# Kernel tuning notes

Measured on AMD Instinct MI355X. Metric: run time of the kernel, lower is better.

## Reference

```python
import jax, jax.numpy as jnp
import numpy as np

BN_EPS = 1e-5

def _l2norm(x, axis):
    # F.normalize: x / max(||x||_2, 1e-12)
    n = jnp.sqrt(jnp.sum(x * x, axis=axis, keepdims=True))
    return x / jnp.maximum(n, 1e-12)

def _psi(x_bhc, w, g, b):
    # 1x1 conv over HW-as-channels: [B,HW,C] x [D,HW] -> [B,D,C]
    y = jnp.einsum('dh,bhc->bdc', w, x_bhc)
    # inference BatchNorm2d with running_mean=0, running_var=1
    scale = g / jnp.sqrt(1.0 + BN_EPS)
    y = y * scale[None, :, None] + b[None, :, None]
    return jax.nn.relu(y)

def setup_inputs() -> dict:
    key = jax.random.key(0)
    ks = jax.random.split(key, 8)
    B, C, H, W, D = 16, 2048, 32, 32, 256
    return {
        'v2l_conv_feature': jax.random.normal(ks[0], (B, C, H, W), jnp.float32),
        'l2v_conv_feature': jax.random.normal(ks[1], (B, C, H, W), jnp.float32),
        'w_v2l': jax.random.normal(ks[2], (D, H * W), jnp.float32) * 0.02,
        'g_v2l': jax.random.uniform(ks[3], (D,), jnp.float32, 0.5, 1.5),
        'b_v2l': jax.random.normal(ks[4], (D,), jnp.float32) * 0.1,
        'w_l2v': jax.random.normal(ks[5], (D, H * W), jnp.float32) * 0.02,
        'g_l2v': jax.random.uniform(ks[6], (D,), jnp.float32, 0.5, 1.5),
        'b_l2v': jax.random.normal(ks[7], (D,), jnp.float32) * 0.1,
    }

def reference(v2l_conv_feature, l2v_conv_feature, w_v2l, g_v2l, b_v2l, w_l2v, g_l2v, b_l2v):
    B, C, H, W = v2l_conv_feature.shape
    HW = H * W
    xv = jnp.transpose(v2l_conv_feature.reshape(B, C, HW), (0, 2, 1))  # [B,HW,C]
    xl = jnp.transpose(l2v_conv_feature.reshape(B, C, HW), (0, 2, 1))  # [B,HW,C]
    v2l_adj = _l2norm(_psi(xv, w_v2l, g_v2l, b_v2l), axis=2)  # [B,D,C], norm over C
    l2v_adj = _l2norm(_psi(xl, w_l2v, g_l2v, b_l2v), axis=1)  # [B,D,C], norm over D
    # Faithful to torch: reshape of the permuted tensor is a raw row-major
    # reinterpretation [B,HW,C] -> [B,C,HW] (NOT a transpose back).
    xv_r = xv.reshape(B, C, HW)
    latent = jnp.einsum('bdc,bch->bdh', v2l_adj, xv_r)          # [B,D,HW]
    latent_n = _l2norm(latent, axis=-1)
    aff = jax.nn.softmax(jnp.einsum('bdh,beh->bde', latent_n, latent_n), axis=-1)  # [B,D,D]
    latent = jnp.einsum('bde,beh->bdh', aff, latent)            # [B,D,HW]
    visible = jnp.einsum('bdc,bdh->bch', l2v_adj, latent)       # [B,C,HW]
    return visible.reshape(B, C, H, W)
```

## Files before the change

### kernel.cpp

```cpp
#include <hip/hip_runtime.h>
#include <hip/hip_bf16.h>

#define BB 16
#define CC 2048
#define HWW 1024
#define DD 256
#define BN_RSQRT 0.9999950000374997f

typedef short bf16x8 __attribute__((ext_vector_type(8)));
typedef float f32x4 __attribute__((ext_vector_type(4)));
typedef unsigned short u16x8 __attribute__((ext_vector_type(8)));
typedef unsigned short u16;

__device__ __forceinline__ unsigned short f2bf(float x) {
    unsigned u = __builtin_bit_cast(unsigned, x);
    unsigned r = u + 0x7FFFu + ((u >> 16) & 1u);
    return (unsigned short)(r >> 16);
}
__device__ __forceinline__ float bf2f(unsigned short h) {
    unsigned u = ((unsigned)h) << 16;
    return __builtin_bit_cast(float, u);
}
__device__ __forceinline__ void split2(float x, unsigned short& hi, unsigned short& lo) {
    hi = f2bf(x);
    lo = f2bf(x - bf2f(hi));
}
__device__ __forceinline__ void split16(const float* v, u16x8& h0, u16x8& h1,
                                        u16x8& l0, u16x8& l1) {
    #pragma unroll
    for (int j = 0; j < 8; ++j) { unsigned short hh, ll; split2(v[j], hh, ll); h0[j] = hh; l0[j] = ll; }
    #pragma unroll
    for (int j = 0; j < 8; ++j) { unsigned short hh, ll; split2(v[8 + j], hh, ll); h1[j] = hh; l1[j] = ll; }
}

struct RegsA { float4 f[4]; u16x8 h[2]; u16x8 l[2]; };
struct RegsB { float4 f[4]; u16x8 h[2]; u16x8 l[2]; };

__global__ __launch_bounds__(256) void split_k(const float* __restrict__ in,
                                               u16* __restrict__ hi, u16* __restrict__ lo,
                                               long long n8) {
    long long i = (long long)blockIdx.x * 256 + threadIdx.x;
    if (i >= n8) return;
    const float4* p = (const float4*)in + i * 2;
    float4 a = p[0], b = p[1];
    float xs[8] = {a.x, a.y, a.z, a.w, b.x, b.y, b.z, b.w};
    u16x8 h, l;
    #pragma unroll
    for (int j = 0; j < 8; ++j) { unsigned short hh, ll; split2(xs[j], hh, ll); h[j] = hh; l[j] = ll; }
    *(u16x8*)(hi + i * 8) = h;
    *(u16x8*)(lo + i * 8) = l;
}

template <int BFMT, int EPI, int FUSE2>
__global__ __launch_bounds__(512, 2) void gemm8(
    const u16* __restrict__ Ah0, const u16* __restrict__ Al0,
    const u16* __restrict__ Ah1, const u16* __restrict__ Al1,
    long long aB, int lda,
    const void* __restrict__ B0a, const void* __restrict__ B0b,
    const void* __restrict__ B1a, const void* __restrict__ B1b,
    long long bB, int ldb,
    float* __restrict__ C0, float* __restrict__ C1, long long cB, int ldc,
    int K,
    const float* __restrict__ g0, const float* __restrict__ bb0,
    const float* __restrict__ g1, const float* __restrict__ bb1)
{
    __shared__ __attribute__((aligned(16))) char smem[2][65536];

    const int gx = gridDim.x, gy = gridDim.y;
    int nwg = gx * gy * gridDim.z;
    int id = blockIdx.x + gx * (blockIdx.y + gy * blockIdx.z);
    int chunk = nwg >> 3;
    int nid = (id & 7) * chunk + (id >> 3);
    int bx = nid % gx;
    int tmp = nid / gx;
    int by = tmp % gy;
    int bz = tmp / gy;

    const int t = threadIdx.x;
    const int n0 = bx * 256, m0 = by * 256;
    const int op = FUSE2 ? (bz >> 4) : 0;
    const int batch = FUSE2 ? (bz & 15) : bz;

    const u16* Ahp = (op ? Ah1 : Ah0) + (long long)batch * aB;
    const u16* Alp = (op ? Al1 : Al0) + (long long)batch * aB;
    const float* Bfp = nullptr;
    const u16* Bhp = nullptr;
    const u16* Blp = nullptr;
    if constexpr (BFMT == 0) {
        Bfp = (const float*)(op ? B1a : B0a) + (long long)batch * bB;
    } else {
        Bhp = (const u16*)(op ? B1a : B0a) + (long long)batch * bB;
        Blp = (const u16*)(op ? B1b : B0b) + (long long)batch * bB;
    }
    float* Cb = (op ? C1 : C0) + (long long)batch * cB;
    const float* gp = op ? g1 : g0;
    const float* bp = op ? bb1 : bb0;

    const int ar = t >> 1, ag = t & 1;
    const int af = (ar >> 1) & 3;
    const int as0 = ((2 * ag) ^ af) * 16, as1 = ((2 * ag + 1) ^ af) * 16;

    const int l = t & 63, w = t >> 6;
    const int wr = w >> 2, wc = w & 3;
    const int rl = l & 15, kq = l >> 4;
    const int sw16 = (kq ^ ((rl >> 1) & 3)) * 16;

    f32x4 acc[8][4];
    #pragma unroll
    for (int i = 0; i < 8; ++i)
        #pragma unroll
        for (int j = 0; j < 4; ++j)
            acc[i][j] = (f32x4){0.f, 0.f, 0.f, 0.f};

    u16x8 rah0, rah1, ral0, ral1;
    u16x8 rbh0, rbh1, rbl0, rbl1;
    float4 rbf0, rbf1, rbf2, rbf3;

    auto loadAB = [&](int k0) {
        const u16* pa = Ahp + (long long)(m0 + ar) * lda + k0 + ag * 16;
        rah0 = *(const u16x8*)pa;
        rah1 = *(const u16x8*)(pa + 8);
        const u16* pl = Alp + (long long)(m0 + ar) * lda + k0 + ag * 16;
        ral0 = *(const u16x8*)pl;
        ral1 = *(const u16x8*)(pl + 8);
        if constexpr (BFMT == 0) {
            const float* pb = Bfp + (long long)(n0 + ar) * ldb + k0 + ag * 16;
            rbf0 = *(const float4*)pb;
            rbf1 = *(const float4*)(pb + 4);
            rbf2 = *(const float4*)(pb + 8);
            rbf3 = *(const float4*)(pb + 12);
        } else {
            const u16* pbh = Bhp + (long long)(n0 + ar) * ldb + k0 + ag * 16;
            rbh0 = *(const u16x8*)pbh;
            rbh1 = *(const u16x8*)(pbh + 8);
            const u16* pbl = Blp + (long long)(n0 + ar) * ldb + k0 + ag * 16;
            rbl0 = *(const u16x8*)pbl;
            rbl1 = *(const u16x8*)(pbl + 8);
        }
    };
    auto writeA = [&](char* sn) {
        char* base = sn + ar * 64;
        *(u16x8*)(base + as0) = rah0;
        *(u16x8*)(base + as1) = rah1;
        *(u16x8*)(base + 16384 + as0) = ral0;
        *(u16x8*)(base + 16384 + as1) = ral1;
    };
    auto writeB = [&](char* sn) {
        char* base = sn + 32768 + ar * 64;
        if constexpr (BFMT == 0) {
            float v[16] = {rbf0.x, rbf0.y, rbf0.z, rbf0.w,
                           rbf1.x, rbf1.y, rbf1.z, rbf1.w,
                           rbf2.x, rbf2.y, rbf2.z, rbf2.w,
                           rbf3.x, rbf3.y, rbf3.z, rbf3.w};
            u16x8 h0, h1, l0, l1;
            split16(v, h0, h1, l0, l1);
            *(u16x8*)(base + as0) = h0;
            *(u16x8*)(base + as1) = h1;
            *(u16x8*)(base + 16384 + as0) = l0;
            *(u16x8*)(base + 16384 + as1) = l1;
        } else {
            *(u16x8*)(base + as0) = rbh0;
            *(u16x8*)(base + as1) = rbh1;
            *(u16x8*)(base + 16384 + as0) = rbl0;
            *(u16x8*)(base + 16384 + as1) = rbl1;
        }
    };

#define PHASE(MH, NH, EXTRA) do {                                              \
    bf16x8 fah[4], fal[4], fbh[2], fbl[2];                                     \
    _Pragma("unroll")                                                          \
    for (int i2 = 0; i2 < 4; ++i2) {                                           \
        int off = (wr * 128 + ((MH) * 4 + i2) * 16 + rl) * 64 + sw16;          \
        fah[i2] = *(const bf16x8*)(sb + off);                                  \
        fal[i2] = *(const bf16x8*)(sb + 16384 + off);                          \
    }                                                                          \
    _Pragma("unroll")                                                          \
    for (int j2 = 0; j2 < 2; ++j2) {                                           \
        int off = (wc * 64 + ((NH) * 2 + j2) * 16 + rl) * 64 + sw16;           \
        fbh[j2] = *(const bf16x8*)(sb + 32768 + off);                          \
        fbl[j2] = *(const bf16x8*)(sb + 49152 + off);                          \
    }                                                                          \
    EXTRA;                                                                     \
    __builtin_amdgcn_s_setprio(1);                                             \
    _Pragma("unroll")                                                          \
    for (int i2 = 0; i2 < 4; ++i2)                                             \
        _Pragma("unroll")                                                      \
        for (int j2 = 0; j2 < 2; ++j2) {                                       \
            f32x4& a = acc[(MH) * 4 + i2][(NH) * 2 + j2];                      \
            a = __builtin_amdgcn_mfma_f32_16x16x32_bf16(fal[i2], fbh[j2], a, 0, 0, 0); \
            a = __builtin_amdgcn_mfma_f32_16x16x32_bf16(fah[i2], fbl[j2], a, 0, 0, 0); \
            a = __builtin_amdgcn_mfma_f32_16x16x32_bf16(fah[i2], fbh[j2], a, 0, 0, 0); \
        }                                                                      \
    __builtin_amdgcn_s_setprio(0);                                             \
} while (0)

    loadAB(0);
    writeA(smem[0]);
    writeB(smem[0]);
    asm volatile("s_waitcnt lgkmcnt(0)" ::: "memory");
    __builtin_amdgcn_s_barrier();

    const int NIT = K >> 5;
    for (int it = 0; it < NIT; ++it) {
        char* sb = smem[it & 1];
        char* sn = smem[(it + 1) & 1];
        const bool more = (it + 1) < NIT;
        const int k1 = (it + 1) << 5;

        PHASE(0, 0, { if (more) loadAB(k1); });
        asm volatile("" ::: "memory");
        __builtin_amdgcn_s_barrier();

        PHASE(0, 1, {});
        asm volatile("" ::: "memory");
        __builtin_amdgcn_s_barrier();

        PHASE(1, 0, { if (more) writeA(sn); });
        asm volatile("" ::: "memory");
        __builtin_amdgcn_s_barrier();

        PHASE(1, 1, { if (more) writeB(sn); });
        asm volatile("s_waitcnt lgkmcnt(0)" ::: "memory");
        __builtin_amdgcn_s_barrier();
    }
#undef PHASE

    #pragma unroll
    for (int i = 0; i < 8; ++i) {
        #pragma unroll
        for (int r = 0; r < 4; ++r) {
            int row = m0 + wr * 128 + i * 16 + kq * 4 + r;
            float sc = 1.0f, bi = 0.0f;
            if (EPI == 1) { sc = gp[row] * BN_RSQRT; bi = bp[row]; }
            #pragma unroll
            for (int j = 0; j < 4; ++j) {
                int col = n0 + wc * 64 + j * 16 + rl;
                float v = acc[i][j][r];
                if (EPI == 1) v = fmaxf(fmaf(v, sc, bi), 0.0f);
                Cb[(long long)row * ldc + col] = v;
            }
        }
    }
}

template <int BN_, int AFMT, int BFMT, int EPI>
__global__ __launch_bounds__(256) void mfma_gemm(
    const void* __restrict__ Ap, const void* __restrict__ Ap2, long long aB, int lda,
    const void* __restrict__ Bp, const void* __restrict__ Bp2, long long bB, int ldb,
    void* __restrict__ Cp, void* __restrict__ Cp2,
    void* __restrict__ Ct, void* __restrict__ Ct2,
    long long cB, int ldc, int ldct,
    int K, const float* __restrict__ gp, const float* __restrict__ bpb)
{
    constexpr int NJ   = BN_ / 32;
    constexpr int BNB  = BN_ * 64;
    constexpr int BUFB = 16384 + BN_ * 128;
    __shared__ __attribute__((aligned(16))) char smem[2][BUFB];

    const int gx = gridDim.x, gy = gridDim.y;
    int nwg = gx * gy * gridDim.z;
    int id = blockIdx.x + gx * (blockIdx.y + gy * blockIdx.z);
    int chunk = nwg >> 3;
    int nid = (id & 7) * chunk + (id >> 3);
    int bx = nid % gx;
    int tmp = nid / gx;
    int by = tmp % gy;
    int bz = tmp / gy;

    const int t  = threadIdx.x;
    const int n0 = bx * BN_;
    const int m0 = by * 128;

    const int ar = t >> 1, ag = t & 1;
    const int af = (ar >> 1) & 3;
    const int as0 = (2 * ag) ^ af, as1 = (2 * ag + 1) ^ af;
    const bool bact = (BN_ == 128) || (t < 2 * BN_);
    const int br = (t >> 1) & (BN_ - 1), bg = t & 1;
    const int bf = (br >> 1) & 3;
    const int bs0 = (2 * bg) ^ bf, bs1 = (2 * bg + 1) ^ bf;

    const int l  = t & 63, w = t >> 6;
    const int wr = w >> 1, wc = w & 1;
    const int rl = l & 15, kq = l >> 4;
    const int sw = kq ^ ((rl >> 1) & 3);
    const int aoff = (wr * 64 + rl) * 64 + sw * 16;
    const int boff = (wc * (BN_ / 2) + rl) * 64 + sw * 16;

    const u16*   Ahp = (const u16*)Ap  + (long long)bz * aB;
    const u16*   Alp = (const u16*)Ap2 + (long long)bz * aB;
    const float* Bfp = (const float*)Bp + (long long)bz * bB;
    const u16*   Bhp = (const u16*)Bp  + (long long)bz * bB;
    const u16*   Blp = (const u16*)Bp2 + (long long)bz * bB;

    auto loadA = [&](int k0, RegsA& ra) {
        const u16* ph = Ahp + (long long)(m0 + ar) * lda + k0 + ag * 16;
        const u16* pl = Alp + (long long)(m0 + ar) * lda + k0 + ag * 16;
        ra.h[0] = *(const u16x8*)(ph);
        ra.h[1] = *(const u16x8*)(ph + 8);
        ra.l[0] = *(const u16x8*)(pl);
        ra.l[1] = *(const u16x8*)(pl + 8);
    };
    auto loadB = [&](int k0, RegsB& rb) {
        if (!bact) return;
        if constexpr (BFMT == 0) {
            const float* p = Bfp + (long long)(n0 + br) * ldb + k0 + bg * 16;
            rb.f[0] = *(const float4*)(p);
            rb.f[1] = *(const float4*)(p + 4);
            rb.f[2] = *(const float4*)(p + 8);
            rb.f[3] = *(const float4*)(p + 12);
        } else if constexpr (BFMT == 1) {
            const u16* ph = Bhp + (long long)(n0 + br) * ldb + k0 + bg * 16;
            const u16* pl = Blp + (long long)(n0 + br) * ldb + k0 + bg * 16;
            rb.h[0] = *(const u16x8*)(ph);
            rb.h[1] = *(const u16x8*)(ph + 8);
            rb.l[0] = *(const u16x8*)(pl);
            rb.l[1] = *(const u16x8*)(pl + 8);
        } else {
            int q0 = (k0 >> 1) + bg * 8;
            const float* p0 = Bfp + (long long)(n0 + br) * HWW + q0;
            const float* p1 = p0 + (long long)HWW * HWW;
            rb.f[0] = *(const float4*)(p0);
            rb.f[1] = *(const float4*)(p0 + 4);
            rb.f[2] = *(const float4*)(p1);
            rb.f[3] = *(const float4*)(p1 + 4);
        }
    };
    auto stageWrite = [&](char* sb, RegsA& ra, RegsB& rb) {
        *(u16x8*)(sb + ar * 64 + as0 * 16) = ra.h[0];
        *(u16x8*)(sb + ar * 64 + as1 * 16) = ra.h[1];
        *(u16x8*)(sb + 8192 + ar * 64 + as0 * 16) = ra.l[0];
        *(u16x8*)(sb + 8192 + ar * 64 + as1 * 16) = ra.l[1];
        if (bact) {
            char* sB = sb + 16384;
            if constexpr (BFMT == 1) {
                *(u16x8*)(sB + br * 64 + bs0 * 16) = rb.h[0];
                *(u16x8*)(sB + br * 64 + bs1 * 16) = rb.h[1];
                *(u16x8*)(sB + BNB + br * 64 + bs0 * 16) = rb.l[0];
                *(u16x8*)(sB + BNB + br * 64 + bs1 * 16) = rb.l[1];
            } else {
                float v[16];
                if constexpr (BFMT == 0) {
                    float vv[16] = {rb.f[0].x, rb.f[0].y, rb.f[0].z, rb.f[0].w,
                                    rb.f[1].x, rb.f[1].y, rb.f[1].z, rb.f[1].w,
                                    rb.f[2].x, rb.f[2].y, rb.f[2].z, rb.f[2].w,
                                    rb.f[3].x, rb.f[3].y, rb.f[3].z, rb.f[3].w};
                    #pragma unroll
                    for (int j = 0; j < 16; ++j) v[j] = vv[j];
                } else {
                    float vv[16] = {rb.f[0].x, rb.f[2].x, rb.f[0].y, rb.f[2].y,
                                    rb.f[0].z, rb.f[2].z, rb.f[0].w, rb.f[2].w,
                                    rb.f[1].x, rb.f[3].x, rb.f[1].y, rb.f[3].y,
                                    rb.f[1].z, rb.f[3].z, rb.f[1].w, rb.f[3].w};
                    #pragma unroll
                    for (int j = 0; j < 16; ++j) v[j] = vv[j];
                }
                u16x8 h0, h1, l0, l1;
                split16(v, h0, h1, l0, l1);
                *(u16x8*)(sB + br * 64 + bs0 * 16) = h0;
                *(u16x8*)(sB + br * 64 + bs1 * 16) = h1;
                *(u16x8*)(sB + BNB + br * 64 + bs0 * 16) = l0;
                *(u16x8*)(sB + BNB + br * 64 + bs1 * 16) = l1;
            }
        }
    };

    f32x4 acc[4][NJ];
    #pragma unroll
    for (int i = 0; i < 4; ++i)
        #pragma unroll
        for (int j = 0; j < NJ; ++j)
            acc[i][j] = (f32x4){0.f, 0.f, 0.f, 0.f};

    RegsA a0, a1;
    RegsB b0, b1;
    const int NIT = K >> 5;

    loadA(0, a0); loadB(0, b0);
    stageWrite(smem[0], a0, b0);
    loadA(32, a1); loadB(32, b1);
    asm volatile("s_waitcnt lgkmcnt(0)" ::: "memory");
    __builtin_amdgcn_s_barrier();

    auto step = [&](int it, char* sb, char* sn, RegsA& pa, RegsB& pb,
                    RegsA& qa, RegsB& qb) {
        bf16x8 fah[4], fal[4], fbh[NJ], fbl[NJ];
        #pragma unroll
        for (int i = 0; i < 4; ++i) {
            fah[i] = *(const bf16x8*)(sb + aoff + i * 1024);
            fal[i] = *(const bf16x8*)(sb + 8192 + aoff + i * 1024);
        }
        #pragma unroll
        for (int j = 0; j < NJ; ++j) {
            fbh[j] = *(const bf16x8*)(sb + 16384 + boff + j * 1024);
            fbl[j] = *(const bf16x8*)(sb + 16384 + BNB + boff + j * 1024);
        }
        if (it + 1 < NIT) stageWrite(sn, pa, pb);
        if (it + 2 < NIT) { loadA((it + 2) << 5, qa); loadB((it + 2) << 5, qb); }
        #pragma unroll
        for (int i = 0; i < 4; ++i)
            #pragma unroll
            for (int j = 0; j < NJ; ++j) {
                acc[i][j] = __builtin_amdgcn_mfma_f32_16x16x32_bf16(fal[i], fbh[j], acc[i][j], 0, 0, 0);
                acc[i][j] = __builtin_amdgcn_mfma_f32_16x16x32_bf16(fah[i], fbl[j], acc[i][j], 0, 0, 0);
                acc[i][j] = __builtin_amdgcn_mfma_f32_16x16x32_bf16(fah[i], fbh[j], acc[i][j], 0, 0, 0);
            }
        asm volatile("s_waitcnt lgkmcnt(0)" ::: "memory");
        __builtin_amdgcn_s_barrier();
    };

    for (int it = 0; it < NIT; it += 2) {
        step(it,     smem[0], smem[1], a1, b1, a0, b0);
        step(it + 1, smem[1], smem[0], a0, b0, a1, b1);
    }

    #pragma unroll
    for (int i = 0; i < 4; ++i) {
        #pragma unroll
        for (int r = 0; r < 4; ++r) {
            int row = m0 + wr * 64 + i * 16 + kq * 4 + r;
            float sc = 1.0f, bi = 0.0f;
            if (EPI == 1) { sc = gp[row] * BN_RSQRT; bi = bpb[row]; }
            #pragma unroll
            for (int j = 0; j < NJ; ++j) {
                int col = n0 + wc * (BN_ / 2) + j * 16 + rl;
                float v = acc[i][j][r];
                if constexpr (EPI == 0) {
                    ((float*)Cp + (long long)bz * cB)[(long long)row * ldc + col] = v;
                } else if constexpr (EPI == 1) {
                    v = fmaxf(fmaf(v, sc, bi), 0.0f);
                    ((float*)Cp + (long long)bz * cB)[(long long)row * ldc + col] = v;
                } else {
                    unsigned short hh, ll; split2(v, hh, ll);
                    ((u16*)Cp  + (long long)bz * cB)[(long long)row * ldc + col] = hh;
                    ((u16*)Cp2 + (long long)bz * cB)[(long long)row * ldc + col] = ll;
                    if constexpr (EPI == 2) {
                        ((u16*)Ct  + (long long)bz * cB)[(long long)col * ldct + row] = hh;
                        ((u16*)Ct2 + (long long)bz * cB)[(long long)col * ldct + row] = ll;
                    }
                }
            }
        }
    }
}

__global__ __launch_bounds__(256) void rownorm_split_k(float* __restrict__ Y) {
    int d = blockIdx.x, b = blockIdx.y, t = threadIdx.x;
    float* row = Y + ((long long)b * DD + d) * CC;
    float4 v0 = ((const float4*)row)[2 * t];
    float4 v1 = ((const float4*)row)[2 * t + 1];
    float s = v0.x * v0.x + v0.y * v0.y + v0.z * v0.z + v0.w * v0.w
            + v1.x * v1.x + v1.y * v1.y + v1.z * v1.z + v1.w * v1.w;
    for (int off = 32; off > 0; off >>= 1) s += __shfl_down(s, off, 64);
    __shared__ float wsum[4];
    __shared__ float ivs;
    int lane = t & 63, w = t >> 6;
    if (lane == 0) wsum[w] = s;
    __syncthreads();
    if (t == 0) ivs = 1.0f / fmaxf(sqrtf(wsum[0] + wsum[1] + wsum[2] + wsum[3]), 1e-12f);
    __syncthreads();
    float iv = ivs;
    float xs[8] = {v0.x * iv, v0.y * iv, v0.z * iv, v0.w * iv,
                   v1.x * iv, v1.y * iv, v1.z * iv, v1.w * iv};
    u16x8 h, l2;
    #pragma unroll
    for (int j = 0; j < 8; ++j) { unsigned short hh, ll; split2(xs[j], hh, ll); h[j] = hh; l2[j] = ll; }
    u16* hi = (u16*)row;
    *(u16x8*)(hi + t * 8) = h;
    *(u16x8*)(hi + CC + t * 8) = l2;
}

__global__ __launch_bounds__(256) void colnorm_k(const float* __restrict__ Yl,
                                                 float* __restrict__ rsc) {
    int b = blockIdx.y;
    int c = blockIdx.x * 256 + threadIdx.x;
    const float* base = Yl + (long long)b * DD * CC + c;
    float s = 0.0f;
    for (int d = 0; d < DD; ++d) { float v = base[(long long)d * CC]; s += v * v; }
    rsc[(long long)b * CC + c] = 1.0f / fmaxf(sqrtf(s), 1e-12f);
}

__global__ __launch_bounds__(256) void trans_split_k(const float* __restrict__ in,
                                                     const float* __restrict__ scale,
                                                     u16* __restrict__ hi, u16* __restrict__ lo) {
    __shared__ float tile[32][33];
    int s0 = blockIdx.x * 32, r0 = blockIdx.y * 32, b = blockIdx.z;
    const float* inb = in + (long long)b * DD * CC;
    int tx = threadIdx.x & 31, ty = threadIdx.x >> 5;
    for (int i = ty; i < 32; i += 8)
        tile[i][tx] = inb[(long long)(r0 + i) * CC + s0 + tx];
    __syncthreads();
    for (int i = ty; i < 32; i += 8) {
        float v = tile[tx][i] * scale[(long long)b * CC + s0 + i];
        unsigned short hh, ll; split2(v, hh, ll);
        long long o = (long long)b * DD * CC + (long long)(s0 + i) * DD + r0 + tx;
        hi[o] = hh; lo[o] = ll;
    }
}

__global__ __launch_bounds__(256) void latnorm_k(const float* __restrict__ G,
                                                 float* __restrict__ rs) {
    int i = blockIdx.x * 256 + threadIdx.x;
    int b = i >> 8, d = i & 255;
    float v = G[((long long)b * DD + d) * DD + d];
    rs[i] = 1.0f / fmaxf(sqrtf(v), 1e-12f);
}

__global__ __launch_bounds__(256) void softmax_k(const float* __restrict__ G,
                                                 const float* __restrict__ rs,
                                                 u16* __restrict__ affHi,
                                                 u16* __restrict__ affLo) {
    int d = blockIdx.x, b = blockIdx.y;
    const float* row = G + ((long long)b * DD + d) * DD;
    const float* rsb = rs + (long long)b * DD;
    int t = threadIdx.x;
    float lg = row[t] * rsb[d] * rsb[t];

    float m = lg;
    for (int off = 32; off > 0; off >>= 1) m = fmaxf(m, __shfl_down(m, off, 64));
    __shared__ float wsm[4];
    __shared__ float bm, bs;
    int lane = t & 63, w = t >> 6;
    if (lane == 0) wsm[w] = m;
    __syncthreads();
    if (t == 0) bm = fmaxf(fmaxf(wsm[0], wsm[1]), fmaxf(wsm[2], wsm[3]));
    __syncthreads();
    float e = expf(lg - bm);
    float s = e;
    for (int off = 32; off > 0; off >>= 1) s += __shfl_down(s, off, 64);
    if (lane == 0) wsm[w] = s;
    __syncthreads();
    if (t == 0) bs = wsm[0] + wsm[1] + wsm[2] + wsm[3];
    __syncthreads();
    float v = e / bs;
    unsigned short hh, ll; split2(v, hh, ll);
    long long o = ((long long)b * DD + d) * DD + t;
    affHi[o] = hh; affLo[o] = ll;
}

extern "C" void kernel_launch(void* const* d_in, const int* in_sizes, int n_in,
                              void* d_out, int out_size, void* d_ws, size_t ws_size,
                              hipStream_t stream) {
    const float* v2l   = (const float*)d_in[0];
    const float* l2v   = (const float*)d_in[1];
    const float* w_v2l = (const float*)d_in[2];
    const float* g_v2l = (const float*)d_in[3];
    const float* b_v2l = (const float*)d_in[4];
    const float* w_l2v = (const float*)d_in[5];
    const float* g_l2v = (const float*)d_in[6];
    const float* b_l2v = (const float*)d_in[7];
    float* out = (float*)d_out;

    char* W = (char*)d_ws;
    float* Yv     = (float*)(W + 0);
    float* Yl     = (float*)(W + 33554432);
    u16*   YltHi  = (u16*)(W + 67108864);
    u16*   YltLo  = (u16*)(W + 83886080);
    u16*   latHi  = (u16*)(W + 100663296);
    u16*   latLo  = (u16*)(W + 109051904);
    u16*   latTHi = (u16*)(W + 117440512);
    u16*   latTLo = (u16*)(W + 125829120);
    u16*   l2tHi  = (u16*)(W + 134217728);
    u16*   l2tLo  = (u16*)(W + 142606336);
    float* gram   = (float*)(W + 150994944);
    float* rs     = (float*)(W + 155189248);
    float* rsc    = (float*)(W + 155205632);
    u16*   affHi  = (u16*)(W + 155336704);
    u16*   affLo  = (u16*)(W + 157433856);
    u16*   WvHi   = (u16*)(W + 159531008);
    u16*   WvLo   = WvHi + 262144;
    u16*   WlHi   = WvLo + 262144;
    u16*   WlLo   = WlHi + 262144;

    const long long sY   = (long long)DD * CC;
    const long long sL   = (long long)DD * HWW;
    const long long sG   = (long long)DD * DD;
    const long long sX   = (long long)CC * HWW;
    const long long sYp  = (long long)DD * 4096;

    split_k<<<128, 256, 0, stream>>>(w_v2l, WvHi, WvLo, 32768);
    split_k<<<128, 256, 0, stream>>>(w_l2v, WlHi, WlLo, 32768);

    gemm8<0, 1, 1><<<dim3(CC / 256, 1, 32), 512, 0, stream>>>(
        WvHi, WvLo, WlHi, WlLo, 0, HWW,
        v2l, nullptr, l2v, nullptr, sX, HWW,
        Yv, Yl, sY, CC, HWW,
        g_v2l, b_v2l, g_l2v, b_l2v);

    rownorm_split_k<<<dim3(DD, BB), 256, 0, stream>>>(Yv);
    colnorm_k<<<dim3(CC / 256, BB), 256, 0, stream>>>(Yl, rsc);
    trans_split_k<<<dim3(CC / 32, DD / 32, BB), 256, 0, stream>>>(Yl, rsc, YltHi, YltLo);

    mfma_gemm<64, 1, 2, 2><<<dim3(HWW / 64, 2, BB), 256, 0, stream>>>(
        (const u16*)Yv, (const u16*)Yv + CC, sYp, 4096, v2l, nullptr, sX, HWW,
        latHi, latLo, latTHi, latTLo, sL, HWW, DD, CC, nullptr, nullptr);

    mfma_gemm<64, 1, 1, 0><<<dim3(4, 2, BB), 256, 0, stream>>>(
        latHi, latLo, sL, HWW, latHi, latLo, sL, HWW,
        gram, nullptr, nullptr, nullptr, sG, DD, 0, HWW, nullptr, nullptr);

    latnorm_k<<<dim3(BB * DD / 256), 256, 0, stream>>>(gram, rs);
    softmax_k<<<dim3(DD, BB), 256, 0, stream>>>(gram, rs, affHi, affLo);

    mfma_gemm<128, 1, 1, 3><<<dim3(2, HWW / 128, BB), 256, 0, stream>>>(
        latTHi, latTLo, sL, DD, affHi, affLo, sG, DD,
        l2tHi, l2tLo, nullptr, nullptr, sL, DD, 0, DD, nullptr, nullptr);

    gemm8<1, 0, 0><<<dim3(HWW / 256, CC / 256, BB), 512, 0, stream>>>(
        YltHi, YltLo, nullptr, nullptr, sY, DD,
        l2tHi, l2tLo, nullptr, nullptr, sL, DD,
        out, nullptr, sX, HWW, DD,
        nullptr, nullptr, nullptr, nullptr);
}
```

Baseline: 403.7 us.

## Route latent GEMM through split-K gemm8 with direct-to-LDS A loads and reduce

The main 256x256 GEMM now loads its A operand straight into LDS through global_load_lds and double-buffers B in registers two iterations ahead, with explicit vmcnt waits. The latent GEMM (D x HW with K=C) moves off the small mfma_gemm onto this kernel. It uses a 4-way split-K grid writing fp32 partials into the output buffer, then a new reduction kernel sums them and emits the hi/lo and transposed splits. The Yv row-norm kernel now writes an even/odd-permuted layout to match the new B-indexing scheme. This adds a partial-sum round-trip through memory and a new launch in exchange for better occupancy and load overlap.

```diff
diff --git a/kernel.cpp b/kernel.cpp
--- a/kernel.cpp
+++ b/kernel.cpp
@@ -10,7 +10,14 @@
 typedef short bf16x8 __attribute__((ext_vector_type(8)));
 typedef float f32x4 __attribute__((ext_vector_type(4)));
 typedef unsigned short u16x8 __attribute__((ext_vector_type(8)));
+typedef unsigned short u16x4 __attribute__((ext_vector_type(4)));
 typedef unsigned short u16;
+
+typedef __attribute__((address_space(1))) const unsigned GU;
+typedef __attribute__((address_space(3))) unsigned LU;
+__device__ __forceinline__ void gload16(const void* g, void* l) {
+    __builtin_amdgcn_global_load_lds((GU*)g, (LU*)l, 16, 0, 0);
+}
 
 __device__ __forceinline__ unsigned short f2bf(float x) {
     unsigned u = __builtin_bit_cast(unsigned, x);
@@ -33,6 +40,7 @@
     for (int j = 0; j < 8; ++j) { unsigned short hh, ll; split2(v[8 + j], hh, ll); h1[j] = hh; l1[j] = ll; }
 }
 
+struct BSet { float4 f0, f1, f2, f3; u16x8 h0, h1, l0, l1; };
 struct RegsA { float4 f[4]; u16x8 h[2]; u16x8 l[2]; };
 struct RegsB { float4 f[4]; u16x8 h[2]; u16x8 l[2]; };
 
@@ -51,7 +59,7 @@
     *(u16x8*)(lo + i * 8) = l;
 }
 
-template <int BFMT, int EPI, int FUSE2>
+template <int BFMT, int EPI, int FUSE2, int KS>
 __global__ __launch_bounds__(512, 2) void gemm8(
     const u16* __restrict__ Ah0, const u16* __restrict__ Al0,
     const u16* __restrict__ Ah1, const u16* __restrict__ Al1,
@@ -59,7 +67,8 @@
     const void* __restrict__ B0a, const void* __restrict__ B0b,
     const void* __restrict__ B1a, const void* __restrict__ B1b,
     long long bB, int ldb,
-    float* __restrict__ C0, float* __restrict__ C1, long long cB, int ldc,
+    float* __restrict__ C0, float* __restrict__ C1,
+    long long cB, long long kB, int ldc,
     int K,
     const float* __restrict__ g0, const float* __restrict__ bb0,
     const float* __restrict__ g1, const float* __restrict__ bb1)
@@ -78,24 +87,33 @@
 
     const int t = threadIdx.x;
     const int n0 = bx * 256, m0 = by * 256;
-    const int op = FUSE2 ? (bz >> 4) : 0;
-    const int batch = FUSE2 ? (bz & 15) : bz;
-
-    const u16* Ahp = (op ? Ah1 : Ah0) + (long long)batch * aB;
-    const u16* Alp = (op ? Al1 : Al0) + (long long)batch * aB;
-    const float* Bfp = nullptr;
-    const u16* Bhp = nullptr;
-    const u16* Blp = nullptr;
-    if constexpr (BFMT == 0) {
-        Bfp = (const float*)(op ? B1a : B0a) + (long long)batch * bB;
+
+    int op = 0, batch, kz = 0;
+    if constexpr (FUSE2) { op = bz >> 4; batch = bz & 15; }
+    else if constexpr (KS > 1) { batch = bz / KS; kz = bz - batch * KS; }
+    else { batch = bz; }
+    const int koff = kz * K;
+
+    const u16* Ahp = (op ? Ah1 : Ah0) + (long long)batch * aB + koff;
+    const u16* Alp = (op ? Al1 : Al0) + (long long)batch * aB + koff;
+    const float* Bf = nullptr;
+    const u16* Bh = nullptr;
+    const u16* Bl = nullptr;
+    if constexpr (BFMT == 1) {
+        Bh = (const u16*)(op ? B1a : B0a) + (long long)batch * bB + koff;
+        Bl = (const u16*)(op ? B1b : B0b) + (long long)batch * bB + koff;
+    } else if constexpr (BFMT == 0) {
+        Bf = (const float*)(op ? B1a : B0a) + (long long)batch * bB + koff;
     } else {
-        Bhp = (const u16*)(op ? B1a : B0a) + (long long)batch * bB;
-        Blp = (const u16*)(op ? B1b : B0b) + (long long)batch * bB;
-    }
-    float* Cb = (op ? C1 : C0) + (long long)batch * cB;
+        Bf = (const float*)B0a + (long long)batch * bB;
+    }
+    float* Cb = ((EPI == 1 && FUSE2) ? (op ? C1 : C0) : C0)
+              + (long long)batch * cB + (long long)kz * kB;
     const float* gp = op ? g1 : g0;
     const float* bp = op ? bb1 : bb0;
 
+    const int grow0 = t >> 2;
+    const int gs0 = ((t & 3) ^ ((grow0 >> 1) & 3)) * 8;
     const int ar = t >> 1, ag = t & 1;
     const int af = (ar >> 1) & 3;
     const int as0 = ((2 * ag) ^ af) * 16, as1 = ((2 * ag + 1) ^ af) * 16;
@@ -112,57 +130,56 @@
         for (int j = 0; j < 4; ++j)
             acc[i][j] = (f32x4){0.f, 0.f, 0.f, 0.f};
 
-    u16x8 rah0, rah1, ral0, ral1;
-    u16x8 rbh0, rbh1, rbl0, rbl1;
-    float4 rbf0, rbf1, rbf2, rbf3;
-
-    auto loadAB = [&](int k0) {
-        const u16* pa = Ahp + (long long)(m0 + ar) * lda + k0 + ag * 16;
-        rah0 = *(const u16x8*)pa;
-        rah1 = *(const u16x8*)(pa + 8);
-        const u16* pl = Alp + (long long)(m0 + ar) * lda + k0 + ag * 16;
-        ral0 = *(const u16x8*)pl;
-        ral1 = *(const u16x8*)(pl + 8);
+    auto gloadA = [&](int k0, char* sn) {
+        const u16* ph = Ahp + (long long)(m0 + grow0) * lda + k0 + gs0;
+        gload16(ph,                           sn + t * 16);
+        gload16(ph + (long long)128 * lda,    sn + 8192 + t * 16);
+        const u16* pl = Alp + (long long)(m0 + grow0) * lda + k0 + gs0;
+        gload16(pl,                           sn + 16384 + t * 16);
+        gload16(pl + (long long)128 * lda,    sn + 24576 + t * 16);
+    };
+    auto loadB = [&](int k0, BSet& s) {
         if constexpr (BFMT == 0) {
-            const float* pb = Bfp + (long long)(n0 + ar) * ldb + k0 + ag * 16;
-            rbf0 = *(const float4*)pb;
-            rbf1 = *(const float4*)(pb + 4);
-            rbf2 = *(const float4*)(pb + 8);
-            rbf3 = *(const float4*)(pb + 12);
+            const float* p = Bf + (long long)(n0 + ar) * ldb + k0 + ag * 16;
+            s.f0 = *(const float4*)(p);
+            s.f1 = *(const float4*)(p + 4);
+            s.f2 = *(const float4*)(p + 8);
+            s.f3 = *(const float4*)(p + 12);
+        } else if constexpr (BFMT == 1) {
+            const u16* ph = Bh + (long long)(n0 + ar) * ldb + k0 + ag * 16;
+            s.h0 = *(const u16x8*)(ph);
+            s.h1 = *(const u16x8*)(ph + 8);
+            const u16* pl = Bl + (long long)(n0 + ar) * ldb + k0 + ag * 16;
+            s.l0 = *(const u16x8*)(pl);
+            s.l1 = *(const u16x8*)(pl + 8);
         } else {
-            const u16* pbh = Bhp + (long long)(n0 + ar) * ldb + k0 + ag * 16;
-            rbh0 = *(const u16x8*)pbh;
-            rbh1 = *(const u16x8*)(pbh + 8);
-            const u16* pbl = Blp + (long long)(n0 + ar) * ldb + k0 + ag * 16;
-            rbl0 = *(const u16x8*)pbl;
-            rbl1 = *(const u16x8*)(pbl + 8);
+            int col = koff + k0 + ag * 16;
+            const float* p = Bf + ((long long)((col >> 10) << 10) + n0 + ar) * ldb
+                           + (col & 1023);
+            s.f0 = *(const float4*)(p);
+            s.f1 = *(const float4*)(p + 4);
+            s.f2 = *(const float4*)(p + 8);
+            s.f3 = *(const float4*)(p + 12);
         }
     };
-    auto writeA = [&](char* sn) {
-        char* base = sn + ar * 64;
-        *(u16x8*)(base + as0) = rah0;
-        *(u16x8*)(base + as1) = rah1;
-        *(u16x8*)(base + 16384 + as0) = ral0;
-        *(u16x8*)(base + 16384 + as1) = ral1;
-    };
-    auto writeB = [&](char* sn) {
+    auto writeB = [&](char* sn, BSet& s) {
         char* base = sn + 32768 + ar * 64;
-        if constexpr (BFMT == 0) {
-            float v[16] = {rbf0.x, rbf0.y, rbf0.z, rbf0.w,
-                           rbf1.x, rbf1.y, rbf1.z, rbf1.w,
-                           rbf2.x, rbf2.y, rbf2.z, rbf2.w,
-                           rbf3.x, rbf3.y, rbf3.z, rbf3.w};
+        if constexpr (BFMT == 1) {
+            *(u16x8*)(base + as0) = s.h0;
+            *(u16x8*)(base + as1) = s.h1;
+            *(u16x8*)(base + 16384 + as0) = s.l0;
+            *(u16x8*)(base + 16384 + as1) = s.l1;
+        } else {
+            float v[16] = {s.f0.x, s.f0.y, s.f0.z, s.f0.w,
+                           s.f1.x, s.f1.y, s.f1.z, s.f1.w,
+                           s.f2.x, s.f2.y, s.f2.z, s.f2.w,
+                           s.f3.x, s.f3.y, s.f3.z, s.f3.w};
             u16x8 h0, h1, l0, l1;
             split16(v, h0, h1, l0, l1);
             *(u16x8*)(base + as0) = h0;
             *(u16x8*)(base + as1) = h1;
             *(u16x8*)(base + 16384 + as0) = l0;
             *(u16x8*)(base + 16384 + as1) = l1;
-        } else {
-            *(u16x8*)(base + as0) = rbh0;
-            *(u16x8*)(base + as1) = rbh1;
-            *(u16x8*)(base + 16384 + as0) = rbl0;
-            *(u16x8*)(base + 16384 + as1) = rbl1;
         }
     };
 
@@ -194,34 +211,47 @@
     __builtin_amdgcn_s_setprio(0);                                             \
 } while (0)
 
-    loadAB(0);
-    writeA(smem[0]);
-    writeB(smem[0]);
+    const int NIT = K >> 5;
+    BSet s0, s1;
+
+    loadB(0, s0);
+    gloadA(0, smem[0]);
+    asm volatile("s_waitcnt vmcnt(4)" ::: "memory");
+    writeB(smem[0], s0);
+    loadB(32, s1);
+    asm volatile("s_waitcnt vmcnt(4)" ::: "memory");
     asm volatile("s_waitcnt lgkmcnt(0)" ::: "memory");
     __builtin_amdgcn_s_barrier();
 
-    const int NIT = K >> 5;
-    for (int it = 0; it < NIT; ++it) {
-        char* sb = smem[it & 1];
-        char* sn = smem[(it + 1) & 1];
-        const bool more = (it + 1) < NIT;
-        const int k1 = (it + 1) << 5;
-
-        PHASE(0, 0, { if (more) loadAB(k1); });
+    auto tile_body = [&](int it, char* sb, char* sn, BSet& sW, BSet& sL) {
+        const bool more1 = (it + 1) < NIT;
+        const bool more2 = (it + 2) < NIT;
+        PHASE(0, 0, { if (more1) gloadA((it + 1) << 5, sn); });
         asm volatile("" ::: "memory");
         __builtin_amdgcn_s_barrier();
 
-        PHASE(0, 1, {});
+        PHASE(0, 1, { if (more2) loadB((it + 2) << 5, sL); });
         asm volatile("" ::: "memory");
         __builtin_amdgcn_s_barrier();
 
-        PHASE(1, 0, { if (more) writeA(sn); });
+        PHASE(1, 0, {
+            if (more2)      { asm volatile("s_waitcnt vmcnt(8)" ::: "memory"); }
+            else if (more1) { asm volatile("s_waitcnt vmcnt(4)" ::: "memory"); }
+            if (more1) writeB(sn, sW);
+        });
         asm volatile("" ::: "memory");
         __builtin_amdgcn_s_barrier();
 
-        PHASE(1, 1, { if (more) writeB(sn); });
+        PHASE(1, 1, {});
+        if (more2)      { asm volatile("s_waitcnt vmcnt(4)" ::: "memory"); }
+        else if (more1) { asm volatile("s_waitcnt vmcnt(0)" ::: "memory"); }
         asm volatile("s_waitcnt lgkmcnt(0)" ::: "memory");
         __builtin_amdgcn_s_barrier();
+    };
+
+    for (int it = 0; it < NIT; it += 2) {
+        tile_body(it,     smem[0], smem[1], s1, s0);
+        tile_body(it + 1, smem[1], smem[0], s0, s1);
     }
 #undef PHASE
 
@@ -288,7 +318,6 @@
 
     const u16*   Ahp = (const u16*)Ap  + (long long)bz * aB;
     const u16*   Alp = (const u16*)Ap2 + (long long)bz * aB;
-    const float* Bfp = (const float*)Bp + (long long)bz * bB;
     const u16*   Bhp = (const u16*)Bp  + (long long)bz * bB;
     const u16*   Blp = (const u16*)Bp2 + (long long)bz * bB;
 
@@ -302,28 +331,12 @@
     };
     auto loadB = [&](int k0, RegsB& rb) {
         if (!bact) return;
-        if constexpr (BFMT == 0) {
-            const float* p = Bfp + (long long)(n0 + br) * ldb + k0 + bg * 16;
-            rb.f[0] = *(const float4*)(p);
-            rb.f[1] = *(const float4*)(p + 4);
-            rb.f[2] = *(const float4*)(p + 8);
-            rb.f[3] = *(const float4*)(p + 12);
-        } else if constexpr (BFMT == 1) {
-            const u16* ph = Bhp + (long long)(n0 + br) * ldb + k0 + bg * 16;
-            const u16* pl = Blp + (long long)(n0 + br) * ldb + k0 + bg * 16;
-            rb.h[0] = *(const u16x8*)(ph);
-            rb.h[1] = *(const u16x8*)(ph + 8);
-            rb.l[0] = *(const u16x8*)(pl);
-            rb.l[1] = *(const u16x8*)(pl + 8);
-        } else {
-            int q0 = (k0 >> 1) + bg * 8;
-            const float* p0 = Bfp + (long long)(n0 + br) * HWW + q0;
-            const float* p1 = p0 + (long long)HWW * HWW;
-            rb.f[0] = *(const float4*)(p0);
-            rb.f[1] = *(const float4*)(p0 + 4);
-            rb.f[2] = *(const float4*)(p1);
-            rb.f[3] = *(const float4*)(p1 + 4);
-        }
+        const u16* ph = Bhp + (long long)(n0 + br) * ldb + k0 + bg * 16;
+        const u16* pl = Blp + (long long)(n0 + br) * ldb + k0 + bg * 16;
+        rb.h[0] = *(const u16x8*)(ph);
+        rb.h[1] = *(const u16x8*)(ph + 8);
+        rb.l[0] = *(const u16x8*)(pl);
+        rb.l[1] = *(const u16x8*)(pl + 8);
     };
     auto stageWrite = [&](char* sb, RegsA& ra, RegsB& rb) {
         *(u16x8*)(sb + ar * 64 + as0 * 16) = ra.h[0];
@@ -332,35 +345,10 @@
         *(u16x8*)(sb + 8192 + ar * 64 + as1 * 16) = ra.l[1];
         if (bact) {
             char* sB = sb + 16384;
-            if constexpr (BFMT == 1) {
-                *(u16x8*)(sB + br * 64 + bs0 * 16) = rb.h[0];
-                *(u16x8*)(sB + br * 64 + bs1 * 16) = rb.h[1];
-                *(u16x8*)(sB + BNB + br * 64 + bs0 * 16) = rb.l[0];
-                *(u16x8*)(sB + BNB + br * 64 + bs1 * 16) = rb.l[1];
-            } else {
-                float v[16];
-                if constexpr (BFMT == 0) {
-                    float vv[16] = {rb.f[0].x, rb.f[0].y, rb.f[0].z, rb.f[0].w,
-                                    rb.f[1].x, rb.f[1].y, rb.f[1].z, rb.f[1].w,
-                                    rb.f[2].x, rb.f[2].y, rb.f[2].z, rb.f[2].w,
-                                    rb.f[3].x, rb.f[3].y, rb.f[3].z, rb.f[3].w};
-                    #pragma unroll
-                    for (int j = 0; j < 16; ++j) v[j] = vv[j];
-                } else {
-                    float vv[16] = {rb.f[0].x, rb.f[2].x, rb.f[0].y, rb.f[2].y,
-                                    rb.f[0].z, rb.f[2].z, rb.f[0].w, rb.f[2].w,
-                                    rb.f[1].x, rb.f[3].x, rb.f[1].y, rb.f[3].y,
-                                    rb.f[1].z, rb.f[3].z, rb.f[1].w, rb.f[3].w};
-                    #pragma unroll
-                    for (int j = 0; j < 16; ++j) v[j] = vv[j];
-                }
-                u16x8 h0, h1, l0, l1;
-                split16(v, h0, h1, l0, l1);
-                *(u16x8*)(sB + br * 64 + bs0 * 16) = h0;
-                *(u16x8*)(sB + br * 64 + bs1 * 16) = h1;
-                *(u16x8*)(sB + BNB + br * 64 + bs0 * 16) = l0;
-                *(u16x8*)(sB + BNB + br * 64 + bs1 * 16) = l1;
-            }
+            *(u16x8*)(sB + br * 64 + bs0 * 16) = rb.h[0];
+            *(u16x8*)(sB + br * 64 + bs1 * 16) = rb.h[1];
+            *(u16x8*)(sB + BNB + br * 64 + bs0 * 16) = rb.l[0];
+            *(u16x8*)(sB + BNB + br * 64 + bs1 * 16) = rb.l[1];
         }
     };
 
@@ -418,32 +406,23 @@
         #pragma unroll
         for (int r = 0; r < 4; ++r) {
             int row = m0 + wr * 64 + i * 16 + kq * 4 + r;
-            float sc = 1.0f, bi = 0.0f;
-            if (EPI == 1) { sc = gp[row] * BN_RSQRT; bi = bpb[row]; }
             #pragma unroll
             for (int j = 0; j < NJ; ++j) {
                 int col = n0 + wc * (BN_ / 2) + j * 16 + rl;
                 float v = acc[i][j][r];
                 if constexpr (EPI == 0) {
                     ((float*)Cp + (long long)bz * cB)[(long long)row * ldc + col] = v;
-                } else if constexpr (EPI == 1) {
-                    v = fmaxf(fmaf(v, sc, bi), 0.0f);
-                    ((float*)Cp + (long long)bz * cB)[(long long)row * ldc + col] = v;
                 } else {
                     unsigned short hh, ll; split2(v, hh, ll);
                     ((u16*)Cp  + (long long)bz * cB)[(long long)row * ldc + col] = hh;
                     ((u16*)Cp2 + (long long)bz * cB)[(long long)row * ldc + col] = ll;
-                    if constexpr (EPI == 2) {
-                        ((u16*)Ct  + (long long)bz * cB)[(long long)col * ldct + row] = hh;
-                        ((u16*)Ct2 + (long long)bz * cB)[(long long)col * ldct + row] = ll;
-                    }
                 }
             }
         }
     }
 }
 
-__global__ __launch_bounds__(256) void rownorm_split_k(float* __restrict__ Y) {
+__global__ __launch_bounds__(256) void rownorm_split_perm_k(float* __restrict__ Y) {
     int d = blockIdx.x, b = blockIdx.y, t = threadIdx.x;
     float* row = Y + ((long long)b * DD + d) * CC;
     float4 v0 = ((const float4*)row)[2 * t];
@@ -461,12 +440,18 @@
     float iv = ivs;
     float xs[8] = {v0.x * iv, v0.y * iv, v0.z * iv, v0.w * iv,
                    v1.x * iv, v1.y * iv, v1.z * iv, v1.w * iv};
-    u16x8 h, l2;
-    #pragma unroll
-    for (int j = 0; j < 8; ++j) { unsigned short hh, ll; split2(xs[j], hh, ll); h[j] = hh; l2[j] = ll; }
+    u16x4 he, ho, le, lo4;
+    #pragma unroll
+    for (int j = 0; j < 4; ++j) {
+        unsigned short hh, ll;
+        split2(xs[2 * j], hh, ll);       he[j] = hh; le[j] = ll;
+        split2(xs[2 * j + 1], hh, ll);   ho[j] = hh; lo4[j] = ll;
+    }
     u16* hi = (u16*)row;
-    *(u16x8*)(hi + t * 8) = h;
-    *(u16x8*)(hi + CC + t * 8) = l2;
+    *(u16x4*)(hi + 4 * t) = he;
+    *(u16x4*)(hi + 1024 + 4 * t) = ho;
+    *(u16x4*)(hi + 2048 + 4 * t) = le;
+    *(u16x4*)(hi + 3072 + 4 * t) = lo4;
 }
 
 __global__ __launch_bounds__(256) void colnorm_k(const float* __restrict__ Yl,
@@ -494,6 +479,32 @@
         unsigned short hh, ll; split2(v, hh, ll);
         long long o = (long long)b * DD * CC + (long long)(s0 + i) * DD + r0 + tx;
         hi[o] = hh; lo[o] = ll;
+    }
+}
+
+__global__ __launch_bounds__(256) void latreduce_k(const float* __restrict__ parts,
+                                                   u16* __restrict__ hi, u16* __restrict__ lo,
+                                                   u16* __restrict__ thi, u16* __restrict__ tlo) {
+    __shared__ float tile[32][33];
+    int h0 = blockIdx.x * 32, d0 = blockIdx.y * 32, b = blockIdx.z;
+    const long long sL = (long long)DD * HWW;
+    const long long ps = (long long)BB * sL;
+    const float* base = parts + (long long)b * sL;
+    int tx = threadIdx.x & 31, ty = threadIdx.x >> 5;
+    for (int i = ty; i < 32; i += 8) {
+        long long o = (long long)(d0 + i) * HWW + h0 + tx;
+        float s = base[o] + base[o + ps] + base[o + 2 * ps] + base[o + 3 * ps];
+        tile[i][tx] = s;
+        unsigned short hh, ll; split2(s, hh, ll);
+        long long od = (long long)b * sL + o;
+        hi[od] = hh; lo[od] = ll;
+    }
+    __syncthreads();
+    for (int i = ty; i < 32; i += 8) {
+        float v = tile[tx][i];
+        unsigned short hh, ll; split2(v, hh, ll);
+        long long ot = (long long)b * sL + (long long)(h0 + i) * DD + d0 + tx;
+        thi[ot] = hh; tlo[ot] = ll;
     }
 }
 
@@ -571,6 +582,8 @@
     u16*   WlHi   = WvLo + 262144;
     u16*   WlLo   = WlHi + 262144;
 
+    float* latPart = (float*)d_out;
+
     const long long sY   = (long long)DD * CC;
     const long long sL   = (long long)DD * HWW;
     const long long sG   = (long long)DD * DD;
@@ -580,19 +593,24 @@
     split_k<<<128, 256, 0, stream>>>(w_v2l, WvHi, WvLo, 32768);
     split_k<<<128, 256, 0, stream>>>(w_l2v, WlHi, WlLo, 32768);
 
-    gemm8<0, 1, 1><<<dim3(CC / 256, 1, 32), 512, 0, stream>>>(
+    gemm8<0, 1, 1, 1><<<dim3(CC / 256, 1, 32), 512, 0, stream>>>(
         WvHi, WvLo, WlHi, WlLo, 0, HWW,
         v2l, nullptr, l2v, nullptr, sX, HWW,
-        Yv, Yl, sY, CC, HWW,
+        Yv, Yl, sY, 0, CC, HWW,
         g_v2l, b_v2l, g_l2v, b_l2v);
 
-    rownorm_split_k<<<dim3(DD, BB), 256, 0, stream>>>(Yv);
+    rownorm_split_perm_k<<<dim3(DD, BB), 256, 0, stream>>>(Yv);
     colnorm_k<<<dim3(CC / 256, BB), 256, 0, stream>>>(Yl, rsc);
     trans_split_k<<<dim3(CC / 32, DD / 32, BB), 256, 0, stream>>>(Yl, rsc, YltHi, YltLo);
 
-    mfma_gemm<64, 1, 2, 2><<<dim3(HWW / 64, 2, BB), 256, 0, stream>>>(
-        (const u16*)Yv, (const u16*)Yv + CC, sYp, 4096, v2l, nullptr, sX, HWW,
-        latHi, latLo, latTHi, latTLo, sL, HWW, DD, CC, nullptr, nullptr);
+    gemm8<3, 0, 0, 4><<<dim3(HWW / 256, 1, 64), 512, 0, stream>>>(
+        (const u16*)Yv, (const u16*)Yv + 2048, nullptr, nullptr, sYp, 4096,
+        v2l, nullptr, nullptr, nullptr, sX, HWW,
+        latPart, nullptr, sL, (long long)BB * sL, HWW, 512,
+        nullptr, nullptr, nullptr, nullptr);
+
+    latreduce_k<<<dim3(HWW / 32, DD / 32, BB), 256, 0, stream>>>(
+        latPart, latHi, latLo, latTHi, latTLo);
 
     mfma_gemm<64, 1, 1, 0><<<dim3(4, 2, BB), 256, 0, stream>>>(
         latHi, latLo, sL, HWW, latHi, latLo, sL, HWW,
@@ -601,13 +619,13 @@
     latnorm_k<<<dim3(BB * DD / 256), 256, 0, stream>>>(gram, rs);
     softmax_k<<<dim3(DD, BB), 256, 0, stream>>>(gram, rs, affHi, affLo);
 
-    mfma_gemm<128, 1, 1, 3><<<dim3(2, HWW / 128, BB), 256, 0, stream>>>(
+    mfma_gemm<128, 1, 1, 3><<<dim3(2, 8, BB), 256, 0, stream>>>(
         latTHi, latTLo, sL, DD, affHi, affLo, sG, DD,
         l2tHi, l2tLo, nullptr, nullptr, sL, DD, 0, DD, nullptr, nullptr);
 
-    gemm8<1, 0, 0><<<dim3(HWW / 256, CC / 256, BB), 512, 0, stream>>>(
+    gemm8<1, 0, 0, 1><<<dim3(HWW / 256, CC / 256, BB), 512, 0, stream>>>(
         YltHi, YltLo, nullptr, nullptr, sY, DD,
         l2tHi, l2tLo, nullptr, nullptr, sL, DD,
-        out, nullptr, sX, HWW, DD,
+        out, nullptr, sX, 0, HWW, DD,
         nullptr, nullptr, nullptr, nullptr);
 }
```

Measured after the change: 430.0 us. 1.07x slower.
